# Performance work log

Hardware: AMD Instinct MI355X
Metric: run time of the kernel (lower is better)

The kernel has to match this reference:

```python
import jax, jax.numpy as jnp
import numpy as np

THETA = 0.5
LEAF_SIZE = 32
N_ATOMS = 8192
N_GRAPHS = 2


def _build_tree(pos_np, indices):
    # Mirrors OpenBoundaryTreeLongRangeKernel._build_tree (octree split at bbox center).
    local = pos_np[indices]
    cmin = local.min(axis=0)
    cmax = local.max(axis=0)
    center = 0.5 * (cmin + cmax)
    half = float((cmax - cmin).max() * 0.5)
    node = {"indices": indices, "iset": set(indices), "center": center,
            "half": half, "children": [], "cid": -1}
    if len(indices) <= LEAF_SIZE:
        return node
    bins = {}
    for i in indices:
        p = pos_np[i]
        key = (int(p[0] >= center[0]), int(p[1] >= center[1]), int(p[2] >= center[2]))
        bins.setdefault(key, []).append(i)
    if len(bins) <= 1:
        return node  # degenerate split -> treated as leaf (is_leaf == no children)
    node["children"] = [_build_tree(pos_np, ci) for ci in bins.values()]
    return node


def _plan(pos_np, batch_np, n_graphs, soft):
    # Host-side Barnes-Hut traversal (the torch original does this with .item() syncs).
    # Emits flat (target, source) direct pairs and (target, cluster) monopole pairs.
    direct_t, direct_s, clus_t, clus_c = [], [], [], []
    clusters = []
    for g in range(n_graphs):
        idx = np.nonzero(batch_np == g)[0]
        if idx.size == 0:
            continue
        root = _build_tree(pos_np, [int(i) for i in idx])
        for t in idx:
            t = int(t)
            tpos = pos_np[t]
            stack = [root]
            while stack:
                node = stack.pop()
                if not node["children"]:  # leaf: direct near-field sum
                    for s in node["indices"]:
                        if s != t:
                            direct_t.append(t)
                            direct_s.append(s)
                    continue
                d = tpos - node["center"]
                dist = float(np.sqrt((d * d).sum() + soft * soft))
                diam = max(2.0 * node["half"], 1e-9)
                if (t not in node["iset"]) and (diam / dist < THETA):
                    if node["cid"] < 0:
                        node["cid"] = len(clusters)
                        clusters.append(node["indices"])
                    clus_t.append(t)
                    clus_c.append(node["cid"])
                else:
                    stack.extend(node["children"])
    if clusters:
        midx = np.concatenate([np.asarray(c, dtype=np.int32) for c in clusters])
        mseg = np.concatenate([np.full(len(c), i, np.int32) for i, c in enumerate(clusters)])
        mcnt = np.asarray([len(c) for c in clusters], dtype=np.float32)
    else:
        midx = np.zeros((0,), np.int32)
        mseg = np.zeros((0,), np.int32)
        mcnt = np.ones((1,), np.float32)
    return (np.asarray(direct_t, np.int32), np.asarray(direct_s, np.int32),
            np.asarray(clus_t, np.int32), np.asarray(clus_c, np.int32),
            midx, mseg, mcnt, max(len(clusters), 1))


def _energy(pos, source, screening, softening, plan, n_atoms):
    # Vectorized, differentiable evaluation of the planned interactions.
    dt, ds, ct, cc, midx, mseg, mcnt, n_clusters = plan
    soft2 = softening * softening
    phi = jnp.zeros((n_atoms,), dtype=pos.dtype)
    if dt.size:
        delta = pos[dt] - pos[ds]                       # [P,3]
        r = jnp.sqrt(jnp.sum(delta * delta, axis=-1) + soft2)
        phi = phi + jax.ops.segment_sum(source[ds] * jnp.exp(-screening * r) / r,
                                        dt, num_segments=n_atoms)
    if ct.size:
        q = jax.ops.segment_sum(source[midx], mseg, num_segments=n_clusters)
        center = (jax.ops.segment_sum(pos[midx], mseg, num_segments=n_clusters)
                  / jnp.asarray(mcnt)[:, None])          # differentiable cluster mean
        delta = pos[ct] - center[cc]                    # [C,3]
        r = jnp.sqrt(jnp.sum(delta * delta, axis=-1) + soft2)
        phi = phi + jax.ops.segment_sum(q[cc] * jnp.exp(-screening * r) / r,
                                        ct, num_segments=n_atoms)
    return 0.5 * (source * phi)[:, None]                # [N,1], energy_partition='potential'


def setup_inputs() -> dict:
    key = jax.random.key(0)
    k1, k2, k3 = jax.random.split(key, 3)
    pos = jax.random.normal(k1, (N_ATOMS, 3), dtype=jnp.float32) * 6.0
    batch = jnp.sort(jax.random.randint(k2, (N_ATOMS,), 0, N_GRAPHS)).astype(jnp.int32)
    cell = jnp.zeros((N_GRAPHS, 3, 3), dtype=jnp.float32)
    source = jax.random.normal(k3, (N_ATOMS,), dtype=jnp.float32)
    screening = jnp.float32(0.5)
    softening = jnp.float32(0.1)
    return {"pos": pos, "batch": batch, "cell": cell, "source": source,
            "screening": screening, "softening": softening}


def reference(pos, batch, cell, source, screening, softening):
    pos_np = np.asarray(pos, dtype=np.float32)
    batch_np = np.asarray(batch)
    plan = _plan(pos_np, batch_np, int(cell.shape[0]), float(np.asarray(softening)))
    return _energy(pos, source, screening, softening, plan, pos.shape[0])
```

## Files before the change

### kernel.cpp

```cpp
#include <hip/hip_runtime.h>

#define LEAF_SZ 32
#define MAXN 16384
#define MAXNODES 65536
#define ARENA_BASE 32768
#define MAXG 64
#define NQ 1024
#define BGRID 128
#define LCAP 256
#define LSTK 192
#define BSTK 32
#define WQCAP 64
#define NW0 16

struct __align__(64) TNode { int4 meta; float4 c4; float4 m4; float4 pad; };

__device__ int    g_perm[MAXN];
__device__ int    g_ptmp[MAXN];
__device__ float4 g_p4[MAXN];
__device__ float4 g_t4[MAXN];
__device__ int    g_nstart[MAXNODES];
__device__ int    g_nend[MAXNODES];
__device__ TNode  g_nodes[MAXNODES];
__device__ int    g_root[MAXG];
__device__ int    g_ncount;
__device__ int    g_lrange[4];
__device__ int    g_done[2];

struct NodeSh {
    float  mn[4][3], mx[4][3];
    double sx[4], sy[4], sz[4], sq[4];
    int    c8[4][8];
    int    cur[8];
    float  cc[3];
    int    info;
    int    base, num;
    int    tot[8], offk[8];
};

__device__ __forceinline__ void process_node2(NodeSh& sh, int n, int st, int en)
{
    const int tid  = threadIdx.x;
    const int wid  = tid >> 6;
    const int lane = tid & 63;
    const int cnt = en - st;

    float mnx = 3.402823466e38f, mny = mnx, mnz = mnx;
    float mxx = -mnx, mxy = -mnx, mxz = -mnx;
    double sx = 0.0, sy = 0.0, sz = 0.0, sq = 0.0;
    for (int j = st + tid; j < en; j += 256) {
        float4 p = g_p4[j];
        mnx = fminf(mnx, p.x); mny = fminf(mny, p.y); mnz = fminf(mnz, p.z);
        mxx = fmaxf(mxx, p.x); mxy = fmaxf(mxy, p.y); mxz = fmaxf(mxz, p.z);
        sx += (double)p.x; sy += (double)p.y; sz += (double)p.z; sq += (double)p.w;
    }
    for (int o = 1; o < 64; o <<= 1) {
        mnx = fminf(mnx, __shfl_xor(mnx, o));
        mny = fminf(mny, __shfl_xor(mny, o));
        mnz = fminf(mnz, __shfl_xor(mnz, o));
        mxx = fmaxf(mxx, __shfl_xor(mxx, o));
        mxy = fmaxf(mxy, __shfl_xor(mxy, o));
        mxz = fmaxf(mxz, __shfl_xor(mxz, o));
        sx += __shfl_xor(sx, o);
        sy += __shfl_xor(sy, o);
        sz += __shfl_xor(sz, o);
        sq += __shfl_xor(sq, o);
    }
    if (lane == 0) {
        sh.mn[wid][0] = mnx; sh.mn[wid][1] = mny; sh.mn[wid][2] = mnz;
        sh.mx[wid][0] = mxx; sh.mx[wid][1] = mxy; sh.mx[wid][2] = mxz;
        sh.sx[wid] = sx; sh.sy[wid] = sy; sh.sz[wid] = sz; sh.sq[wid] = sq;
    }
    __syncthreads();
    if (tid == 0) {
        float a0 = sh.mn[0][0], a1 = sh.mn[0][1], a2 = sh.mn[0][2];
        float b0 = sh.mx[0][0], b1 = sh.mx[0][1], b2 = sh.mx[0][2];
        double tx = sh.sx[0], ty = sh.sy[0], tz = sh.sz[0], tq = sh.sq[0];
        for (int w = 1; w < 4; ++w) {
            a0 = fminf(a0, sh.mn[w][0]); a1 = fminf(a1, sh.mn[w][1]); a2 = fminf(a2, sh.mn[w][2]);
            b0 = fmaxf(b0, sh.mx[w][0]); b1 = fmaxf(b1, sh.mx[w][1]); b2 = fmaxf(b2, sh.mx[w][2]);
            tx += sh.sx[w]; ty += sh.sy[w]; tz += sh.sz[w]; tq += sh.sq[w];
        }
        float cx = 0.5f * (a0 + b0), cy = 0.5f * (a1 + b1), cz = 0.5f * (a2 + b2);
        g_nodes[n].c4 = make_float4(cx, cy, cz, 0.5f * fmaxf(fmaxf(b0 - a0, b1 - a1), b2 - a2));
        const float fc = (float)cnt;
        g_nodes[n].m4 = make_float4((float)tx / fc, (float)ty / fc, (float)tz / fc, (float)tq);
        sh.cc[0] = cx; sh.cc[1] = cy; sh.cc[2] = cz;
        if (cnt <= LEAF_SZ) { g_nodes[n].meta = make_int4(st, en, 0, 0); sh.info = -1; }
        else sh.info = 0;
    }
    __syncthreads();
    if (sh.info < 0) return;
    const float cx = sh.cc[0], cy = sh.cc[1], cz = sh.cc[2];

    int c8[8] = {0,0,0,0,0,0,0,0};
    for (int j = st + tid; j < en; j += 256) {
        float4 p = g_p4[j];
        int oct = (p.x >= cx ? 1 : 0) | (p.y >= cy ? 2 : 0) | (p.z >= cz ? 4 : 0);
        c8[oct]++;
    }
    #pragma unroll
    for (int k = 0; k < 8; ++k)
        for (int o = 1; o < 64; o <<= 1)
            c8[k] += __shfl_xor(c8[k], o);
    if (lane == 0)
        #pragma unroll
        for (int k = 0; k < 8; ++k) sh.c8[wid][k] = c8[k];
    __syncthreads();
    if (tid == 0) {
        int tot[8], nonempty = 0;
        #pragma unroll
        for (int k = 0; k < 8; ++k) {
            tot[k] = sh.c8[0][k] + sh.c8[1][k] + sh.c8[2][k] + sh.c8[3][k];
            nonempty += (tot[k] > 0) ? 1 : 0;
        }
        if (nonempty <= 1) { g_nodes[n].meta = make_int4(st, en, 0, 0); sh.info = -1; }
        else {
            int base = atomicAdd(&g_ncount, nonempty);
            int acc = st, ci = base;
            #pragma unroll
            for (int k = 0; k < 8; ++k) {
                sh.cur[k] = acc;
                sh.offk[k] = acc - st;
                sh.tot[k] = tot[k];
                if (tot[k] > 0) { g_nstart[ci] = acc; g_nend[ci] = acc + tot[k]; ++ci; }
                acc += tot[k];
            }
            g_nodes[n].meta = make_int4(st, en, base, nonempty);
            sh.base = base; sh.num = nonempty; sh.info = 1;
        }
    }
    __syncthreads();
    if (sh.info < 0) return;

    for (int j = st + tid; j < en; j += 256) {
        float4 p = g_p4[j];
        int id = g_perm[j];
        int oct = (p.x >= cx ? 1 : 0) | (p.y >= cy ? 2 : 0) | (p.z >= cz ? 4 : 0);
        int pdst = atomicAdd(&sh.cur[oct], 1);
        g_ptmp[pdst] = id; g_t4[pdst] = p;
    }
    __syncthreads();
    for (int j = st + tid; j < en; j += 256) {
        g_perm[j] = g_ptmp[j];
        g_p4[j]   = g_t4[j];
    }
    __syncthreads();
}

__global__ __launch_bounds__(1024)
void level0_kernel(const float* __restrict__ pos, const float* __restrict__ src,
                   const int* __restrict__ batch, int N, int n_graphs)
{
    __shared__ int    s_first[MAXG], s_end[MAXG];
    __shared__ float  s_mn[NW0][3], s_mx[NW0][3];
    __shared__ double s_sx[NW0], s_sy[NW0], s_sz[NW0], s_sq[NW0];
    __shared__ int    s_c8[NW0][8];
    __shared__ int    s_cur[8];
    __shared__ float  s_cc[3];
    __shared__ int    s_info;
    const int tid = threadIdx.x, wid = tid >> 6, lane = tid & 63;
    const int ng = (n_graphs < MAXG) ? n_graphs : MAXG;

    for (int g = tid; g < MAXG; g += 1024) { s_first[g] = -1; s_end[g] = 0; }
    __syncthreads();
    for (int i = tid; i < N; i += 1024) {
        int b = batch[i];
        if (i == 0     || batch[i-1] != b) s_first[b] = i;
        if (i == N - 1 || batch[i+1] != b) s_end[b]   = i + 1;
    }
    __syncthreads();

    const int g = blockIdx.x;
    int nc = 0, myroot = -1;
    for (int q = 0; q < ng; ++q)
        if (s_first[q] >= 0) { if (q == g) myroot = nc; ++nc; }
    const int nb = nc + 8 * ng;

    if (g == 0 && tid == 0) {
        int r = 0;
        for (int q = 0; q < ng; ++q) {
            if (s_first[q] >= 0) g_root[q] = r++;
            else {
                g_root[q] = -1;
                for (int c = 0; c < 8; ++c) g_nstart[nc + q*8 + c] = -1;
            }
        }
        g_ncount = nb;
        g_lrange[0] = nc;
        g_lrange[1] = nb;
        g_done[1] = 0;
    }
    if (g >= ng || myroot < 0) return;

    const int st = s_first[g], en = s_end[g];
    const int cnt = en - st;
    const int n = myroot;
    const int cbase = nc + g * 8;

    float mnx = 3.402823466e38f, mny = mnx, mnz = mnx;
    float mxx = -mnx, mxy = -mnx, mxz = -mnx;
    double sx = 0.0, sy = 0.0, sz = 0.0, sq = 0.0;
    for (int j = st + tid; j < en; j += 1024) {
        float x = pos[3*j], y = pos[3*j+1], z = pos[3*j+2], s = src[j];
        mnx = fminf(mnx, x); mny = fminf(mny, y); mnz = fminf(mnz, z);
        mxx = fmaxf(mxx, x); mxy = fmaxf(mxy, y); mxz = fmaxf(mxz, z);
        sx += (double)x; sy += (double)y; sz += (double)z; sq += (double)s;
    }
    for (int o = 1; o < 64; o <<= 1) {
        mnx = fminf(mnx, __shfl_xor(mnx, o));
        mny = fminf(mny, __shfl_xor(mny, o));
        mnz = fminf(mnz, __shfl_xor(mnz, o));
        mxx = fmaxf(mxx, __shfl_xor(mxx, o));
        mxy = fmaxf(mxy, __shfl_xor(mxy, o));
        mxz = fmaxf(mxz, __shfl_xor(mxz, o));
        sx += __shfl_xor(sx, o);
        sy += __shfl_xor(sy, o);
        sz += __shfl_xor(sz, o);
        sq += __shfl_xor(sq, o);
    }
    if (lane == 0) {
        s_mn[wid][0] = mnx; s_mn[wid][1] = mny; s_mn[wid][2] = mnz;
        s_mx[wid][0] = mxx; s_mx[wid][1] = mxy; s_mx[wid][2] = mxz;
        s_sx[wid] = sx; s_sy[wid] = sy; s_sz[wid] = sz; s_sq[wid] = sq;
    }
    __syncthreads();
    if (tid == 0) {
        float a0 = s_mn[0][0], a1 = s_mn[0][1], a2 = s_mn[0][2];
        float b0 = s_mx[0][0], b1 = s_mx[0][1], b2 = s_mx[0][2];
        double tx = s_sx[0], ty = s_sy[0], tz = s_sz[0], tq = s_sq[0];
        for (int w = 1; w < NW0; ++w) {
            a0 = fminf(a0, s_mn[w][0]); a1 = fminf(a1, s_mn[w][1]); a2 = fminf(a2, s_mn[w][2]);
            b0 = fmaxf(b0, s_mx[w][0]); b1 = fmaxf(b1, s_mx[w][1]); b2 = fmaxf(b2, s_mx[w][2]);
            tx += s_sx[w]; ty += s_sy[w]; tz += s_sz[w]; tq += s_sq[w];
        }
        float cx = 0.5f * (a0 + b0), cy = 0.5f * (a1 + b1), cz = 0.5f * (a2 + b2);
        g_nodes[n].c4 = make_float4(cx, cy, cz, 0.5f * fmaxf(fmaxf(b0 - a0, b1 - a1), b2 - a2));
        const float fc = (float)cnt;
        g_nodes[n].m4 = make_float4((float)tx / fc, (float)ty / fc, (float)tz / fc, (float)tq);
        s_cc[0] = cx; s_cc[1] = cy; s_cc[2] = cz;
        s_info = (cnt <= LEAF_SZ) ? -1 : 0;
        if (s_info < 0) g_nodes[n].meta = make_int4(st, en, 0, 0);
    }
    __syncthreads();

    if (s_info == 0) {
        const float cx = s_cc[0], cy = s_cc[1], cz = s_cc[2];
        int c8[8] = {0,0,0,0,0,0,0,0};
        for (int j = st + tid; j < en; j += 1024) {
            int oct = (pos[3*j] >= cx ? 1 : 0) | (pos[3*j+1] >= cy ? 2 : 0) | (pos[3*j+2] >= cz ? 4 : 0);
            c8[oct]++;
        }
        #pragma unroll
        for (int k = 0; k < 8; ++k)
            for (int o = 1; o < 64; o <<= 1)
                c8[k] += __shfl_xor(c8[k], o);
        if (lane == 0)
            #pragma unroll
            for (int k = 0; k < 8; ++k) s_c8[wid][k] = c8[k];
        __syncthreads();
        if (tid == 0) {
            int tot[8], nonempty = 0;
            #pragma unroll
            for (int k = 0; k < 8; ++k) {
                int tk = 0;
                for (int w = 0; w < NW0; ++w) tk += s_c8[w][k];
                tot[k] = tk;
                nonempty += (tk > 0) ? 1 : 0;
            }
            if (nonempty <= 1) {
                g_nodes[n].meta = make_int4(st, en, 0, 0);
                for (int c = 0; c < 8; ++c) g_nstart[cbase + c] = -1;
                s_info = -1;
            } else {
                int acc = st, ci = cbase;
                #pragma unroll
                for (int k = 0; k < 8; ++k) {
                    s_cur[k] = acc;
                    if (tot[k] > 0) { g_nstart[ci] = acc; g_nend[ci] = acc + tot[k]; ++ci; }
                    acc += tot[k];
                }
                for (int c = ci; c < cbase + 8; ++c) g_nstart[c] = -1;
                g_nodes[n].meta = make_int4(st, en, cbase, nonempty);
                s_info = 1;
            }
        }
        __syncthreads();
    } else if (tid == 0) {
        for (int c = 0; c < 8; ++c) g_nstart[cbase + c] = -1;
    }

    if (s_info == 1) {
        const float cx = s_cc[0], cy = s_cc[1], cz = s_cc[2];
        for (int j = st + tid; j < en; j += 1024) {
            float x = pos[3*j], y = pos[3*j+1], z = pos[3*j+2], s = src[j];
            int oct = (x >= cx ? 1 : 0) | (y >= cy ? 2 : 0) | (z >= cz ? 4 : 0);
            int pdst = atomicAdd(&s_cur[oct], 1);
            g_p4[pdst] = make_float4(x, y, z, s);
            g_perm[pdst] = j;
        }
    } else {
        for (int j = st + tid; j < en; j += 1024) {
            g_p4[j] = make_float4(pos[3*j], pos[3*j+1], pos[3*j+2], src[j]);
            g_perm[j] = j;
        }
    }
}

__global__ __launch_bounds__(256) void level1_kernel()
{
    __shared__ NodeSh sh;
    const int lb = g_lrange[0], le = g_lrange[1];
    for (int n = lb + blockIdx.x; n < le; n += BGRID) {
        __syncthreads();
        int st = g_nstart[n];
        if (st < 0) continue;
        process_node2(sh, n, st, g_nend[n]);
    }
    __syncthreads();
    if (threadIdx.x == 0) {
        __threadfence();
        int d = atomicAdd(&g_done[1], 1);
        if (d == BGRID - 1)
            g_lrange[2] = atomicAdd(&g_ncount, 0);
    }
}

__device__ __forceinline__ void lds_subtree(int rootn, int st, int en, int abase,
                                            float4* a4, int* aid,
                                            int* lid, int* la, int* lbb)
{
    const int lane = threadIdx.x & 63;
    const int cnt = en - st;
    const unsigned long long mlt = (1ull << lane) - 1ull;

    for (int j = lane; j < cnt; j += 64) {
        a4[j]  = g_p4[st + j];
        aid[j] = g_perm[st + j];
    }
    asm volatile("s_waitcnt vmcnt(0) lgkmcnt(0)" ::: "memory");
    __builtin_amdgcn_wave_barrier();

    int sp = 0;
    int cn = rootn, ca = 0, cb = cnt;
    while (true) {
        const int c = cb - ca;
        float4 pv[4]; int idv[4]; int oc[4];
        float mnx = 3.402823466e38f, mny = mnx, mnz = mnx;
        float mxx = -mnx, mxy = -mnx, mxz = -mnx;
        float sx = 0.f, sy = 0.f, sz = 0.f, sq = 0.f;
        #pragma unroll
        for (int i = 0; i < 4; ++i) {
            bool act = (i*64 + lane) < c;
            int j = act ? (ca + i*64 + lane) : ca;
            float4 p = a4[j];
            pv[i] = p; idv[i] = aid[j];
            if (act) {
                mnx = fminf(mnx, p.x); mny = fminf(mny, p.y); mnz = fminf(mnz, p.z);
                mxx = fmaxf(mxx, p.x); mxy = fmaxf(mxy, p.y); mxz = fmaxf(mxz, p.z);
                sx += p.x; sy += p.y; sz += p.z; sq += p.w;
            }
        }
        for (int o = 1; o < 64; o <<= 1) {
            mnx = fminf(mnx, __shfl_xor(mnx, o));
            mny = fminf(mny, __shfl_xor(mny, o));
            mnz = fminf(mnz, __shfl_xor(mnz, o));
            mxx = fmaxf(mxx, __shfl_xor(mxx, o));
            mxy = fmaxf(mxy, __shfl_xor(mxy, o));
            mxz = fmaxf(mxz, __shfl_xor(mxz, o));
            sx += __shfl_xor(sx, o);
            sy += __shfl_xor(sy, o);
            sz += __shfl_xor(sz, o);
            sq += __shfl_xor(sq, o);
        }
        const float cx = 0.5f * (mnx + mxx);
        const float cy = 0.5f * (mny + mxy);
        const float cz = 0.5f * (mnz + mxz);
        if (lane == 0) {
            g_nodes[cn].c4 = make_float4(cx, cy, cz, 0.5f * fmaxf(fmaxf(mxx - mnx, mxy - mny), mxz - mnz));
            const float fc = (float)c;
            g_nodes[cn].m4 = make_float4(sx / fc, sy / fc, sz / fc, sq);
        }

        int nonempty = 0;
        int c8[8] = {0,0,0,0,0,0,0,0};
        if (c > LEAF_SZ) {
            #pragma unroll
            for (int i = 0; i < 4; ++i) {
                bool act = (i*64 + lane) < c;
                int o = act ? ((pv[i].x >= cx ? 1 : 0) | (pv[i].y >= cy ? 2 : 0) | (pv[i].z >= cz ? 4 : 0)) : 8;
                oc[i] = o;
                #pragma unroll
                for (int k = 0; k < 8; ++k)
                    c8[k] += (int)__popcll(__ballot(o == k));
            }
            #pragma unroll
            for (int k = 0; k < 8; ++k) nonempty += (c8[k] > 0) ? 1 : 0;
        }

        if (c <= LEAF_SZ || nonempty <= 1) {
            if (lane == 0) g_nodes[cn].meta = make_int4(st + ca, st + cb, 0, 0);
        } else {
            int off[8], acc = 0;
            #pragma unroll
            for (int k = 0; k < 8; ++k) { off[k] = acc; acc += c8[k]; }
            if (lane == 0) g_nodes[cn].meta = make_int4(st + ca, st + cb, abase, nonempty);
            int cum[8] = {0,0,0,0,0,0,0,0};
            #pragma unroll
            for (int i = 0; i < 4; ++i) {
                int o = oc[i];
                int pdst = 0;
                #pragma unroll
                for (int k = 0; k < 8; ++k) {
                    unsigned long long b = __ballot(o == k);
                    if (o == k) pdst = ca + off[k] + cum[k] + (int)__popcll(b & mlt);
                    cum[k] += (int)__popcll(b);
                }
                if (o < 8) { a4[pdst] = pv[i]; aid[pdst] = idv[i]; }
            }
            asm volatile("s_waitcnt lgkmcnt(0)" ::: "memory");
            __builtin_amdgcn_wave_barrier();
            if (lane == 0) {
                int ci = 0;
                #pragma unroll
                for (int k = 0; k < 8; ++k) {
                    if (c8[k] > 0) {
                        lid[sp + ci] = abase + ci;
                        la [sp + ci] = ca + off[k];
                        lbb[sp + ci] = ca + off[k] + c8[k];
                        ++ci;
                    }
                }
            }
            abase += nonempty; sp += nonempty;
            if (sp > LSTK) sp = LSTK;
        }
        if (sp <= 0) break;
        --sp;
        __builtin_amdgcn_wave_barrier();
        asm volatile("s_waitcnt lgkmcnt(0)" ::: "memory");
        cn = lid[sp]; ca = la[sp]; cb = lbb[sp];
        __builtin_amdgcn_wave_barrier();
    }

    for (int j = lane; j < cnt; j += 64) {
        g_p4[st + j]  = a4[j];
        g_perm[st + j] = aid[j];
    }
    asm volatile("s_waitcnt vmcnt(0)" ::: "memory");
}

__global__ __launch_bounds__(256) void block_subtree_kernel()
{
    __shared__ NodeSh sh;
    __shared__ int bs_id[BSTK], bs_st[BSTK], bs_en[BSTK];
    __shared__ int wq_id[WQCAP], wq_st[WQCAP], wq_en[WQCAP];
    __shared__ int s_bsp, s_wq;
    __shared__ float4 s_a4[4][LCAP];
    __shared__ int    s_aid[4][LCAP];
    __shared__ int    s_lid[4][LSTK], s_la[4][LSTK], s_lb[4][LSTK];

    const int tid = threadIdx.x;
    const int wid = tid >> 6;
    const int lb = g_lrange[1], le = g_lrange[2];

    for (int task = lb + blockIdx.x; task < le; task += BGRID) {
        __syncthreads();
        if (tid == 0) {
            int st = g_nstart[task], en = g_nend[task];
            if (en - st <= LCAP) { wq_id[0] = task; wq_st[0] = st; wq_en[0] = en; s_wq = 1; s_bsp = 0; }
            else                 { bs_id[0] = task; bs_st[0] = st; bs_en[0] = en; s_bsp = 1; s_wq = 0; }
        }
        __syncthreads();

        while (true) {
            __syncthreads();
            const int bsp = s_bsp;
            if (bsp == 0) break;
            const int n  = bs_id[bsp-1];
            const int st = bs_st[bsp-1];
            const int en = bs_en[bsp-1];
            __syncthreads();
            if (tid == 0) s_bsp = bsp - 1;
            process_node2(sh, n, st, en);
            if (tid == 0 && sh.info == 1) {
                int ci = 0;
                #pragma unroll
                for (int k = 0; k < 8; ++k) {
                    if (sh.tot[k] > 0) {
                        int cst = st + sh.offk[k], cen = cst + sh.tot[k];
                        int cid = sh.base + ci; ++ci;
                        if (cen - cst <= LCAP) {
                            if (s_wq < WQCAP) { wq_id[s_wq] = cid; wq_st[s_wq] = cst; wq_en[s_wq] = cen; ++s_wq; }
                        } else {
                            if (s_bsp < BSTK) { bs_id[s_bsp] = cid; bs_st[s_bsp] = cst; bs_en[s_bsp] = cen; ++s_bsp; }
                        }
                    }
                }
            }
        }
        __syncthreads();

        const int nwq = s_wq;
        float4* a4 = s_a4[wid];  int* aid = s_aid[wid];
        int* lid = s_lid[wid];   int* la = s_la[wid];  int* lbb = s_lb[wid];
        for (int i = wid; i < nwq; i += 4) {
            int cid = wq_id[i], cst = wq_st[i], cen = wq_en[i];
            lds_subtree(cid, cst, cen, ARENA_BASE + 2 * cst, a4, aid, lid, la, lbb);
        }
    }
}

__global__ __launch_bounds__(64)
void traverse_kernel(const int* __restrict__ batch,
                     const float* __restrict__ p_scr, const float* __restrict__ p_soft,
                     float* __restrict__ out, int N)
{
    __shared__ int s_q[NQ];
    __shared__ int s_sb[64], s_ss[64], s_mk[64];
    __shared__ int s_qt;
    const int lane = threadIdx.x & 63;
    const int slot = blockIdx.x;
    if (slot >= N) return;
    const int t = g_perm[slot];

    const float scr   = p_scr[0];
    const float soft  = p_soft[0];
    const float soft2 = soft * soft;
    const float cexp  = -scr * 1.4426950408889634f;
    const float4 tp = g_p4[slot];
    const float tx = tp.x, ty = tp.y, tz = tp.z;
    const int inv_t = slot;

    volatile int* q = s_q;
    if (lane == 0) { q[0] = g_root[batch[t]]; s_qt = 1; }
    __builtin_amdgcn_wave_barrier();

    float phi = 0.f;
    int qh = 0;
    while (true) {
        __builtin_amdgcn_wave_barrier();
        int qt = *(volatile int*)&s_qt;
        if (qh >= qt) break;
        int take = qt - qh; if (take > 64) take = 64;
        int node = (lane < take) ? q[(qh + lane) & (NQ - 1)] : -1;
        qh += take;

        int leaf_st = 0, leaf_cnt = 0;
        if (node >= 0) {
            const int4 meta = g_nodes[node].meta;
            if (meta.w == 0) {
                leaf_st = meta.x; leaf_cnt = meta.y - meta.x;
            } else {
                float4 c4 = g_nodes[node].c4;
                float dx = tx - c4.x, dy = ty - c4.y, dz = tz - c4.z;
                float dist = sqrtf(dx*dx + dy*dy + dz*dz + soft2);
                float diam = fmaxf(2.0f * c4.w, 1e-9f);
                bool inside = (inv_t >= meta.x) && (inv_t < meta.y);
                if (!inside && diam < 0.5f * dist) {
                    float4 m4 = g_nodes[node].m4;
                    float ax = tx - m4.x, ay = ty - m4.y, az = tz - m4.z;
                    float s = ax*ax + ay*ay + az*az + soft2;
                    float rinv = rsqrtf(s);
                    phi += m4.w * exp2f(cexp * (s * rinv)) * rinv;
                } else {
                    int p = atomicAdd(&s_qt, meta.w);
                    for (int c = 0; c < meta.w; ++c) q[(p + c) & (NQ - 1)] = meta.z + c;
                }
            }
        }

        bool hasself = (inv_t >= leaf_st) && (inv_t < leaf_st + leaf_cnt);
        int cnt_adj = leaf_cnt - (hasself ? 1 : 0);
        int x = cnt_adj;
        #pragma unroll
        for (int o = 1; o < 64; o <<= 1) { int y = __shfl_up(x, o); if (lane >= o) x += y; }
        int total = __shfl(x, 63);
        int off = x - cnt_adj;

        if (total > 0) {
            s_sb[lane] = leaf_st - off;
            s_ss[lane] = hasself ? (off + (inv_t - leaf_st)) : 0x7fffffff;
            asm volatile("s_waitcnt lgkmcnt(0)" ::: "memory");
            __builtin_amdgcn_wave_barrier();
            int carry = -1;
            for (int cb = 0; cb < total; cb += 64) {
                s_mk[lane] = -1;
                asm volatile("s_waitcnt lgkmcnt(0)" ::: "memory");
                __builtin_amdgcn_wave_barrier();
                if (cnt_adj > 0 && off >= cb && off < cb + 64) s_mk[off - cb] = lane;
                asm volatile("s_waitcnt lgkmcnt(0)" ::: "memory");
                __builtin_amdgcn_wave_barrier();
                int own = s_mk[lane];
                if (lane == 0) own = own > carry ? own : carry;
                #pragma unroll
                for (int o = 1; o < 64; o <<= 1) {
                    int y = __shfl_up(own, o);
                    if (lane >= o) own = own > y ? own : y;
                }
                carry = __shfl(own, 63);
                int p = cb + lane;
                if (p < total) {
                    int j = s_sb[own] + p + ((p >= s_ss[own]) ? 1 : 0);
                    float4 pp = g_p4[j];
                    float dx = tx - pp.x, dy = ty - pp.y, dz = tz - pp.z;
                    float s = dx*dx + dy*dy + dz*dz + soft2;
                    float rinv = rsqrtf(s);
                    phi += pp.w * exp2f(cexp * (s * rinv)) * rinv;
                }
                __builtin_amdgcn_wave_barrier();
            }
        }
    }

    #pragma unroll
    for (int o = 1; o < 64; o <<= 1) phi += __shfl_xor(phi, o);
    if (lane == 0) out[t] = 0.5f * (tp.w * phi);
}

extern "C" void kernel_launch(void* const* d_in, const int* in_sizes, int n_in,
                              void* d_out, int out_size, void* d_ws, size_t ws_size,
                              hipStream_t stream) {
    const float* pos    = (const float*)d_in[0];
    const int*   batch  = (const int*)  d_in[1];
    const float* source = (const float*)d_in[3];
    const float* p_scr  = (const float*)d_in[4];
    const float* p_soft = (const float*)d_in[5];

    const int N        = in_sizes[0] / 3;
    const int n_graphs = in_sizes[2] / 9;

    int g0 = n_graphs > 0 ? n_graphs : 1;
    if (g0 > MAXG) g0 = MAXG;
    level0_kernel<<<g0, 1024, 0, stream>>>(pos, source, batch, N, n_graphs);
    level1_kernel<<<BGRID, 256, 0, stream>>>();
    block_subtree_kernel<<<BGRID, 256, 0, stream>>>();

    traverse_kernel<<<N, 64, 0, stream>>>(batch, p_scr, p_soft, (float*)d_out, N);
}
```

Before: 154.0 us.

## Traverse tree per group of 32 targets with shared masked BFS queue

Replaces the one-wave-per-target traversal with blocks of 256 threads that process 32 spatially adjacent targets together. Nodes are kept in a level-synchronous shared-memory queue carrying a bitmask of which targets still need to open each node. Four waves pull nodes from the queue dynamically. For leaves, source particles are loaded once and broadcast by shuffle to all masked target lanes. This amortizes node fetches and traversal overhead across targets, but only 32 of 64 lanes do useful work. The shared queue of up to 10240 entries can overflow and silently drop children, and level barriers add synchronisation.

```diff
diff --git a/kernel.cpp b/kernel.cpp
--- a/kernel.cpp
+++ b/kernel.cpp
@@ -5,13 +5,14 @@
 #define MAXNODES 65536
 #define ARENA_BASE 32768
 #define MAXG 64
-#define NQ 1024
 #define BGRID 128
 #define LCAP 256
 #define LSTK 192
 #define BSTK 32
 #define WQCAP 64
 #define NW0 16
+#define QCAP 10240
+#define TGT 32
 
 struct __align__(64) TNode { int4 meta; float4 c4; float4 m4; float4 pad; };
 
@@ -511,111 +512,135 @@
     }
 }
 
-__global__ __launch_bounds__(64)
+__global__ __launch_bounds__(256)
 void traverse_kernel(const int* __restrict__ batch,
                      const float* __restrict__ p_scr, const float* __restrict__ p_soft,
                      float* __restrict__ out, int N)
 {
-    __shared__ int s_q[NQ];
-    __shared__ int s_sb[64], s_ss[64], s_mk[64];
-    __shared__ int s_qt;
-    const int lane = threadIdx.x & 63;
-    const int slot = blockIdx.x;
-    if (slot >= N) return;
-    const int t = g_perm[slot];
+    __shared__ int          s_qn[QCAP];
+    __shared__ unsigned int s_qm[QCAP];
+    __shared__ float        s_phi[4][TGT];
+    __shared__ int s_tail, s_claim, s_lvl_start, s_lvl_end;
+
+    const int tid  = threadIdx.x;
+    const int wid  = tid >> 6;
+    const int lane = tid & 63;
+    const int slot = blockIdx.x * TGT + lane;
+    const bool isT = (lane < TGT) && (slot < N);
 
     const float scr   = p_scr[0];
     const float soft  = p_soft[0];
     const float soft2 = soft * soft;
     const float cexp  = -scr * 1.4426950408889634f;
-    const float4 tp = g_p4[slot];
-    const float tx = tp.x, ty = tp.y, tz = tp.z;
-    const int inv_t = slot;
-
-    volatile int* q = s_q;
-    if (lane == 0) { q[0] = g_root[batch[t]]; s_qt = 1; }
-    __builtin_amdgcn_wave_barrier();
+
+    float tx = 0.f, ty = 0.f, tz = 0.f;
+    if (isT) {
+        float4 tp = g_p4[slot];
+        tx = tp.x; ty = tp.y; tz = tp.z;
+    }
+
+    if (wid == 0) {
+        int r = isT ? g_root[batch[g_perm[slot]]] : -1;
+        unsigned long long rem = __ballot(isT);
+        int ntail = 0;
+        while (rem) {
+            int l = (int)__builtin_ctzll(rem);
+            int rv = __shfl(r, l);
+            unsigned long long m = __ballot(isT && r == rv);
+            if (lane == 0) { s_qn[ntail] = rv; s_qm[ntail] = (unsigned int)m; }
+            ++ntail;
+            rem &= ~m;
+        }
+        if (lane == 0) { s_tail = ntail; s_lvl_start = 0; }
+    }
 
     float phi = 0.f;
-    int qh = 0;
+    __syncthreads();
+
     while (true) {
-        __builtin_amdgcn_wave_barrier();
-        int qt = *(volatile int*)&s_qt;
-        if (qh >= qt) break;
-        int take = qt - qh; if (take > 64) take = 64;
-        int node = (lane < take) ? q[(qh + lane) & (NQ - 1)] : -1;
-        qh += take;
-
-        int leaf_st = 0, leaf_cnt = 0;
-        if (node >= 0) {
-            const int4 meta = g_nodes[node].meta;
+        if (tid == 0) {
+            int tl = s_tail; if (tl > QCAP) tl = QCAP;
+            s_lvl_end = tl;
+            s_claim   = s_lvl_start;
+        }
+        __syncthreads();
+        const int lstart = s_lvl_start, lend = s_lvl_end;
+        if (lstart >= lend) break;
+
+        while (true) {
+            int i = 0;
+            if (lane == 0) i = atomicAdd(&s_claim, 1);
+            i = __shfl(i, 0);
+            if (i >= lend) break;
+
+            const int n = s_qn[i];
+            const unsigned int mask = s_qm[i];
+            const bool mbit = (lane < TGT) ? (((mask >> lane) & 1u) != 0) : false;
+            const int4 meta = g_nodes[n].meta;
+
             if (meta.w == 0) {
-                leaf_st = meta.x; leaf_cnt = meta.y - meta.x;
+                const int lst = meta.x, lcnt = meta.y - meta.x;
+                for (int kb = 0; kb < lcnt; kb += 64) {
+                    const int rem2 = lcnt - kb;
+                    float4 pp = make_float4(0.f, 0.f, 0.f, 0.f);
+                    if (lane < rem2) pp = g_p4[lst + kb + lane];
+                    const int lim = rem2 < 64 ? rem2 : 64;
+                    for (int k = 0; k < lim; ++k) {
+                        float bx = __shfl(pp.x, k);
+                        float by = __shfl(pp.y, k);
+                        float bz = __shfl(pp.z, k);
+                        float bw = __shfl(pp.w, k);
+                        int j = lst + kb + k;
+                        if (mbit && j != slot) {
+                            float dx = tx - bx, dy = ty - by, dz = tz - bz;
+                            float s = dx*dx + dy*dy + dz*dz + soft2;
+                            float rinv = rsqrtf(s);
+                            phi += bw * exp2f(cexp * (s * rinv)) * rinv;
+                        }
+                    }
+                }
             } else {
-                float4 c4 = g_nodes[node].c4;
+                const float4 c4 = g_nodes[n].c4;
+                const float4 m4 = g_nodes[n].m4;
                 float dx = tx - c4.x, dy = ty - c4.y, dz = tz - c4.z;
                 float dist = sqrtf(dx*dx + dy*dy + dz*dz + soft2);
                 float diam = fmaxf(2.0f * c4.w, 1e-9f);
-                bool inside = (inv_t >= meta.x) && (inv_t < meta.y);
-                if (!inside && diam < 0.5f * dist) {
-                    float4 m4 = g_nodes[node].m4;
+                bool inside = (slot >= meta.x) && (slot < meta.y);
+                bool accept = mbit && !inside && (diam < 0.5f * dist);
+                if (accept) {
                     float ax = tx - m4.x, ay = ty - m4.y, az = tz - m4.z;
                     float s = ax*ax + ay*ay + az*az + soft2;
                     float rinv = rsqrtf(s);
                     phi += m4.w * exp2f(cexp * (s * rinv)) * rinv;
-                } else {
-                    int p = atomicAdd(&s_qt, meta.w);
-                    for (int c = 0; c < meta.w; ++c) q[(p + c) & (NQ - 1)] = meta.z + c;
                 }
-            }
-        }
-
-        bool hasself = (inv_t >= leaf_st) && (inv_t < leaf_st + leaf_cnt);
-        int cnt_adj = leaf_cnt - (hasself ? 1 : 0);
-        int x = cnt_adj;
-        #pragma unroll
-        for (int o = 1; o < 64; o <<= 1) { int y = __shfl_up(x, o); if (lane >= o) x += y; }
-        int total = __shfl(x, 63);
-        int off = x - cnt_adj;
-
-        if (total > 0) {
-            s_sb[lane] = leaf_st - off;
-            s_ss[lane] = hasself ? (off + (inv_t - leaf_st)) : 0x7fffffff;
-            asm volatile("s_waitcnt lgkmcnt(0)" ::: "memory");
-            __builtin_amdgcn_wave_barrier();
-            int carry = -1;
-            for (int cb = 0; cb < total; cb += 64) {
-                s_mk[lane] = -1;
-                asm volatile("s_waitcnt lgkmcnt(0)" ::: "memory");
-                __builtin_amdgcn_wave_barrier();
-                if (cnt_adj > 0 && off >= cb && off < cb + 64) s_mk[off - cb] = lane;
-                asm volatile("s_waitcnt lgkmcnt(0)" ::: "memory");
-                __builtin_amdgcn_wave_barrier();
-                int own = s_mk[lane];
-                if (lane == 0) own = own > carry ? own : carry;
-                #pragma unroll
-                for (int o = 1; o < 64; o <<= 1) {
-                    int y = __shfl_up(own, o);
-                    if (lane >= o) own = own > y ? own : y;
+                unsigned long long db = __ballot(mbit && !accept);
+                unsigned int dm = (unsigned int)db;
+                if (dm) {
+                    int b = 0;
+                    if (lane == 0) b = atomicAdd(&s_tail, meta.w);
+                    b = __shfl(b, 0);
+                    if (b + meta.w <= QCAP && lane < meta.w) {
+                        s_qn[b + lane] = meta.z + lane;
+                        s_qm[b + lane] = dm;
+                    }
                 }
-                carry = __shfl(own, 63);
-                int p = cb + lane;
-                if (p < total) {
-                    int j = s_sb[own] + p + ((p >= s_ss[own]) ? 1 : 0);
-                    float4 pp = g_p4[j];
-                    float dx = tx - pp.x, dy = ty - pp.y, dz = tz - pp.z;
-                    float s = dx*dx + dy*dy + dz*dz + soft2;
-                    float rinv = rsqrtf(s);
-                    phi += pp.w * exp2f(cexp * (s * rinv)) * rinv;
-                }
-                __builtin_amdgcn_wave_barrier();
-            }
-        }
-    }
-
-    #pragma unroll
-    for (int o = 1; o < 64; o <<= 1) phi += __shfl_xor(phi, o);
-    if (lane == 0) out[t] = 0.5f * (tp.w * phi);
+            }
+        }
+        __syncthreads();
+        if (tid == 0) s_lvl_start = lend;
+        __syncthreads();
+    }
+
+    if (lane < TGT) s_phi[wid][lane] = phi;
+    __syncthreads();
+    if (tid < TGT) {
+        int sl = blockIdx.x * TGT + tid;
+        if (sl < N) {
+            float sum = s_phi[0][tid] + s_phi[1][tid] + s_phi[2][tid] + s_phi[3][tid];
+            float4 tpp = g_p4[sl];
+            out[g_perm[sl]] = 0.5f * (tpp.w * sum);
+        }
+    }
 }
 
 extern "C" void kernel_launch(void* const* d_in, const int* in_sizes, int n_in,
@@ -636,5 +661,6 @@
     level1_kernel<<<BGRID, 256, 0, stream>>>();
     block_subtree_kernel<<<BGRID, 256, 0, stream>>>();
 
-    traverse_kernel<<<N, 64, 0, stream>>>(batch, p_scr, p_soft, (float*)d_out, N);
+    const int tblocks = (N + TGT - 1) / TGT;
+    traverse_kernel<<<tblocks, 256, 0, stream>>>(batch, p_scr, p_soft, (float*)d_out, N);
 }
```

New measurement: 310.5 us. +101.6%, slower.
